# Kernel optimization log

Measured on AMD Instinct MI355X. Metric: run time of the kernel, lower is better.

The kernel has to match this reference:

```python
import jax, jax.numpy as jnp
import numpy as np

NUM_NODES = 116
EMBED = 64
HIDDEN = 64
OUT_FEAT = 116


def mish(x):
    return x * jnp.tanh(jax.nn.softplus(x))


def sage_conv(x, src, dst, w_l, b_l, w_r, n):
    # PyG SAGEConv (mean aggr): out = lin_l(mean_{j->i} x_j) + lin_r(x_i)
    agg = jax.ops.segment_sum(x[src], dst, num_segments=n)
    cnt = jax.ops.segment_sum(jnp.ones((src.shape[0],), x.dtype), dst, num_segments=n)
    mean = agg / jnp.clip(cnt, 1.0)[:, None]
    return mean @ w_l.T + b_l + x @ w_r.T


def setup_inputs() -> dict:
    key = jax.random.key(0)
    ks = jax.random.split(key, 12)
    B = 64
    N = B * NUM_NODES          # 7424 total nodes
    E = N * 32                 # 237568 edges
    d_in = EMBED * NUM_NODES   # 7424
    d_hid = HIDDEN * NUM_NODES # 7424
    d_out = OUT_FEAT * NUM_NODES  # 13456

    def lin_w(k, fan_out, fan_in):
        s = 1.0 / np.sqrt(fan_in)
        return jax.random.uniform(k, (fan_out, fan_in), jnp.float32, -s, s)

    return {
        "z": jax.random.normal(ks[0], (N, EMBED), jnp.float32),
        "edge_index": jax.random.randint(ks[1], (2, E), 0, N, jnp.int64),
        "batch_size": B,
        "w1_l": lin_w(ks[2], EMBED, EMBED),
        "b1_l": jnp.zeros((EMBED,), jnp.float32),
        "w1_r": lin_w(ks[3], EMBED, EMBED),
        "w2_l": lin_w(ks[4], EMBED, EMBED),
        "b2_l": jnp.zeros((EMBED,), jnp.float32),
        "w2_r": lin_w(ks[5], EMBED, EMBED),
        "fc1_w": lin_w(ks[6], d_hid, d_in),
        "fc1_b": jax.random.uniform(ks[7], (d_hid,), jnp.float32, -1/np.sqrt(d_in), 1/np.sqrt(d_in)),
        "fc2_w": lin_w(ks[8], d_out, d_hid),
        "fc2_b": jax.random.uniform(ks[9], (d_out,), jnp.float32, -1/np.sqrt(d_hid), 1/np.sqrt(d_hid)),
    }


def reference(z, edge_index, batch_size, w1_l, b1_l, w1_r, w2_l, b2_l, w2_r,
              fc1_w, fc1_b, fc2_w, fc2_b):
    n = z.shape[0]
    src, dst = edge_index[0], edge_index[1]
    h = mish(sage_conv(z, src, dst, w1_l, b1_l, w1_r, n))
    h = mish(sage_conv(h, src, dst, w2_l, b2_l, w2_r, n))
    h_flat = h.reshape(batch_size, NUM_NODES * EMBED)
    hidden = mish(h_flat @ fc1_w.T + fc1_b)
    x_rec = (hidden @ fc2_w.T + fc2_b).reshape(batch_size, NUM_NODES, OUT_FEAT)
    # enforce symmetry, unit diagonal
    sym = 0.5 * (x_rec + jnp.swapaxes(x_rec, 1, 2))
    eye = jnp.eye(NUM_NODES, dtype=bool)[None]
    sym = jnp.where(eye, jnp.asarray(1.0, sym.dtype), sym)
    return sym.reshape(batch_size * NUM_NODES, OUT_FEAT)
```

## Files before the change

kernel.cpp:

```cpp
#include <hip/hip_runtime.h>
#include <math.h>

#define NODES_TOT 7424
#define EDGES     237568
#define BATCH     64
#define NN        116
#define KDIM      7424
#define N1        7424
#define N2        13456
#define KSPLIT    8
#define NKB       116

typedef __attribute__((ext_vector_type(8))) short bf16x8;
typedef __attribute__((ext_vector_type(4))) float f32x4;
typedef __attribute__((ext_vector_type(4))) short s16x4;

__device__ __forceinline__ float mish_f(float v) {
    float sp = fmaxf(v, 0.0f) + log1pf(expf(-fabsf(v)));
    return v * tanhf(sp);
}

__device__ __forceinline__ unsigned short bf_rne(float f) {
    unsigned u = __float_as_uint(f);
    u += 0x7fffu + ((u >> 16) & 1u);
    return (unsigned short)(u >> 16);
}

__global__ void zero_kernel(int* __restrict__ p, int n) {
    int i = blockIdx.x * 256 + threadIdx.x;
    if (i < n) p[i] = 0;
}

__global__ void hist_kernel(const int* __restrict__ dst, int* __restrict__ hist) {
    int e = blockIdx.x * 256 + threadIdx.x;
    if (e < EDGES) atomicAdd(&hist[dst[e]], 1);
}

__global__ void scan_kernel(const int* __restrict__ hist, int* __restrict__ row_start,
                            int* __restrict__ cursor) {
    __shared__ int s[1024];
    int t = threadIdx.x;
    int base = t * 8;
    int loc[8];
    int sum = 0;
    #pragma unroll
    for (int c = 0; c < 8; ++c) {
        int idx = base + c;
        int v = (idx < NODES_TOT) ? hist[idx] : 0;
        loc[c] = sum;
        sum += v;
    }
    s[t] = sum;
    __syncthreads();
    for (int off = 1; off < 1024; off <<= 1) {
        int v = (t >= off) ? s[t - off] : 0;
        __syncthreads();
        s[t] += v;
        __syncthreads();
    }
    int excl = s[t] - sum;
    #pragma unroll
    for (int c = 0; c < 8; ++c) {
        int idx = base + c;
        if (idx < NODES_TOT) {
            int r = excl + loc[c];
            row_start[idx] = r;
            cursor[idx] = r;
        }
    }
}

__global__ void csr_fill_kernel(const int* __restrict__ src, const int* __restrict__ dst,
                                int* __restrict__ cursor, int* __restrict__ csr_src) {
    int e = blockIdx.x * 256 + threadIdx.x;
    if (e < EDGES) {
        int p = atomicAdd(&cursor[dst[e]], 1);
        csr_src[p] = src[e];
    }
}

template <bool BF>
__global__ void __launch_bounds__(256) conv_kernel(
        const float* __restrict__ x, const int* __restrict__ csr_src,
        const int* __restrict__ row_start, const int* __restrict__ deg_arr,
        const float* __restrict__ w_l, const float* __restrict__ b_l,
        const float* __restrict__ w_r, void* __restrict__ h_out_v) {
    __shared__ float wlT[64 * 64];
    __shared__ float wrT[64 * 64];
    __shared__ float mv[4][64];
    __shared__ float xv[4][64];
    int t = threadIdx.x;
    for (int i = 0; i < 16; ++i) {
        int idx = t + i * 256;
        int f = idx >> 6, k = idx & 63;
        wlT[k * 64 + f] = w_l[idx];
        wrT[k * 64 + f] = w_r[idx];
    }
    int g = t >> 6, f = t & 63;
    __syncthreads();
    for (int nb = blockIdx.x * 4; nb < NODES_TOT; nb += gridDim.x * 4) {
        int node = nb + g;
        int deg = deg_arr[node];
        int rs = row_start[node];
        float sum = 0.f;
        for (int e = 0; e < deg; ++e) {
            int s = csr_src[rs + e];
            sum += x[s * 64 + f];
        }
        float mean = sum / (float)max(deg, 1);
        mv[g][f] = mean;
        xv[g][f] = x[node * 64 + f];
        __syncthreads();
        float o = b_l[f];
        #pragma unroll
        for (int k = 0; k < 64; ++k) {
            o = fmaf(mv[g][k], wlT[k * 64 + f], o);
            o = fmaf(xv[g][k], wrT[k * 64 + f], o);
        }
        float m = mish_f(o);
        if (BF) ((unsigned short*)h_out_v)[node * 64 + f] = bf_rne(m);
        else    ((float*)h_out_v)[node * 64 + f] = m;
        __syncthreads();
    }
}

__global__ void __launch_bounds__(256) gemm_tile(
        const unsigned short* __restrict__ Abf, const float* __restrict__ W,
        float* __restrict__ Cp, int N) {
    __shared__ __align__(16) short Whi[512 * 8];
    __shared__ __align__(16) short Wlo[512 * 8];
    __shared__ __align__(16) short Ash[512 * 8];
    int t = threadIdx.x;
    int bx = blockIdx.x, by = blockIdx.y;
    int kb0 = (by * NKB) >> 3;
    int kb1 = ((by + 1) * NKB) >> 3;
    int n0 = bx * 64;
    int srow = t >> 2;
    int scq = t & 3;
    int wr = n0 + srow; if (wr >= N) wr = N - 1;
    const float* wsrc = W + (size_t)wr * KDIM + scq * 16;
    const unsigned short* asrc = Abf + (size_t)srow * KDIM + scq * 16;
    int f0 = scq * 2, f1 = f0 + 1;
    int c0 = (f0 * 64 + (srow ^ (f0 & 7))) * 8;
    int c1 = (f1 * 64 + (srow ^ (f1 & 7))) * 8;
    int wv = t >> 6, l = t & 63, l15 = l & 15, hi = l >> 4;
    f32x4 acc[4];
    #pragma unroll
    for (int g = 0; g < 4; ++g) acc[g] = (f32x4){0.f, 0.f, 0.f, 0.f};

    size_t k0 = (size_t)kb0 * 64;
    f32x4 w0 = *(const f32x4*)(wsrc + k0);
    f32x4 w1 = *(const f32x4*)(wsrc + k0 + 4);
    f32x4 w2 = *(const f32x4*)(wsrc + k0 + 8);
    f32x4 w3 = *(const f32x4*)(wsrc + k0 + 12);
    bf16x8 a0 = *(const bf16x8*)(asrc + k0);
    bf16x8 a1 = *(const bf16x8*)(asrc + k0 + 8);

    for (int kb = kb0; kb < kb1; ++kb) {
        bf16x8 h0, l0, h1, l1;
        #pragma unroll
        for (int j = 0; j < 4; ++j) {
            float fv = w0[j];
            unsigned short h = bf_rne(fv);
            h0[j] = (short)h;
            l0[j] = (short)bf_rne(fv - __uint_as_float((unsigned)h << 16));
            fv = w1[j];
            h = bf_rne(fv);
            h0[4 + j] = (short)h;
            l0[4 + j] = (short)bf_rne(fv - __uint_as_float((unsigned)h << 16));
            fv = w2[j];
            h = bf_rne(fv);
            h1[j] = (short)h;
            l1[j] = (short)bf_rne(fv - __uint_as_float((unsigned)h << 16));
            fv = w3[j];
            h = bf_rne(fv);
            h1[4 + j] = (short)h;
            l1[4 + j] = (short)bf_rne(fv - __uint_as_float((unsigned)h << 16));
        }
        __syncthreads();
        *(bf16x8*)&Whi[c0] = h0;
        *(bf16x8*)&Wlo[c0] = l0;
        *(bf16x8*)&Whi[c1] = h1;
        *(bf16x8*)&Wlo[c1] = l1;
        *(bf16x8*)&Ash[c0] = a0;
        *(bf16x8*)&Ash[c1] = a1;
        __syncthreads();
        if (kb + 1 < kb1) {
            size_t kn = (size_t)(kb + 1) * 64;
            w0 = *(const f32x4*)(wsrc + kn);
            w1 = *(const f32x4*)(wsrc + kn + 4);
            w2 = *(const f32x4*)(wsrc + kn + 8);
            w3 = *(const f32x4*)(wsrc + kn + 12);
            a0 = *(const bf16x8*)(asrc + kn);
            a1 = *(const bf16x8*)(asrc + kn + 8);
        }
        #pragma unroll
        for (int s = 0; s < 2; ++s) {
            int fw = s * 4 + hi;
            int wc = (fw * 64 + ((wv * 16 + l15) ^ (fw & 7))) * 8;
            bf16x8 bh = *(const bf16x8*)&Whi[wc];
            bf16x8 bl = *(const bf16x8*)&Wlo[wc];
            #pragma unroll
            for (int g = 0; g < 4; ++g) {
                int ac = (fw * 64 + ((g * 16 + l15) ^ (fw & 7))) * 8;
                bf16x8 av = *(const bf16x8*)&Ash[ac];
                acc[g] = __builtin_amdgcn_mfma_f32_16x16x32_bf16(av, bh, acc[g], 0, 0, 0);
                acc[g] = __builtin_amdgcn_mfma_f32_16x16x32_bf16(av, bl, acc[g], 0, 0, 0);
            }
        }
    }
    int gn = n0 + wv * 16 + l15;
    if (gn < N) {
        float* cp = Cp + (size_t)by * 64 * N;
        #pragma unroll
        for (int g = 0; g < 4; ++g)
            #pragma unroll
            for (int r = 0; r < 4; ++r)
                cp[(size_t)(g * 16 + hi * 4 + r) * N + gn] = acc[g][r];
    }
}

__global__ void reduce1_kernel(const float* __restrict__ Cp, const float* __restrict__ b,
                               unsigned short* __restrict__ A2) {
    int i4 = (blockIdx.x * 256 + threadIdx.x) * 4;
    if (i4 >= BATCH * N1) return;
    int n = i4 % N1;
    f32x4 acc = *(const f32x4*)(b + n);
    #pragma unroll
    for (int s = 0; s < KSPLIT; ++s)
        acc += *(const f32x4*)(Cp + (size_t)s * BATCH * N1 + i4);
    s16x4 o;
    #pragma unroll
    for (int j = 0; j < 4; ++j) o[j] = (short)bf_rne(mish_f(acc[j]));
    *(s16x4*)(A2 + i4) = o;
}

__global__ void reduce2_kernel(const float* __restrict__ Cp, const float* __restrict__ b,
                               float* __restrict__ C2) {
    int i4 = (blockIdx.x * 256 + threadIdx.x) * 4;
    if (i4 >= BATCH * N2) return;
    int n = i4 % N2;
    f32x4 acc = *(const f32x4*)(b + n);
    #pragma unroll
    for (int s = 0; s < KSPLIT; ++s)
        acc += *(const f32x4*)(Cp + (size_t)s * BATCH * N2 + i4);
    *(f32x4*)(C2 + i4) = acc;
}

__global__ void sym_kernel(const float* __restrict__ C2, float* __restrict__ out) {
    int tid = blockIdx.x * 256 + threadIdx.x;
    if (tid >= BATCH * NN * NN) return;
    int j = tid % NN;
    int r = tid / NN;
    int i = r % NN;
    int b = r / NN;
    float v;
    if (i == j) {
        v = 1.0f;
    } else {
        v = 0.5f * (C2[(size_t)b * N2 + i * NN + j] + C2[(size_t)b * N2 + j * NN + i]);
    }
    out[tid] = v;
}

extern "C" void kernel_launch(void* const* d_in, const int* in_sizes, int n_in,
                              void* d_out, int out_size, void* d_ws, size_t ws_size,
                              hipStream_t stream) {
    const float* z     = (const float*)d_in[0];
    const int*   edge  = (const int*)d_in[1];
    const float* w1_l  = (const float*)d_in[3];
    const float* b1_l  = (const float*)d_in[4];
    const float* w1_r  = (const float*)d_in[5];
    const float* w2_l  = (const float*)d_in[6];
    const float* b2_l  = (const float*)d_in[7];
    const float* w2_r  = (const float*)d_in[8];
    const float* fc1_w = (const float*)d_in[9];
    const float* fc1_b = (const float*)d_in[10];
    const float* fc2_w = (const float*)d_in[11];
    const float* fc2_b = (const float*)d_in[12];
    float* out = (float*)d_out;

    char* ws = (char*)d_ws;
    size_t off = 0;
    auto alloc = [&](size_t bytes) {
        void* p = ws + off;
        off = (off + bytes + 255) & ~(size_t)255;
        return p;
    };
    int*            hist      = (int*)alloc(NODES_TOT * 4);
    int*            row_start = (int*)alloc(NODES_TOT * 4);
    int*            cursor    = (int*)alloc(NODES_TOT * 4);
    int*            csr_src   = (int*)alloc((size_t)EDGES * 4);
    float*          h1        = (float*)alloc((size_t)NODES_TOT * 64 * 4);
    unsigned short* A1        = (unsigned short*)alloc((size_t)NODES_TOT * 64 * 2);
    float*          Cp1       = (float*)alloc((size_t)KSPLIT * BATCH * N1 * 4);
    unsigned short* A2        = (unsigned short*)alloc((size_t)BATCH * N1 * 2);
    float*          Cp2       = (float*)alloc((size_t)KSPLIT * BATCH * N2 * 4);
    float*          C2        = (float*)alloc((size_t)BATCH * N2 * 4);

    const int* src = edge;
    const int* dst = edge + EDGES;

    zero_kernel<<<(NODES_TOT + 255) / 256, 256, 0, stream>>>(hist, NODES_TOT);
    hist_kernel<<<(EDGES + 255) / 256, 256, 0, stream>>>(dst, hist);
    scan_kernel<<<1, 1024, 0, stream>>>(hist, row_start, cursor);
    csr_fill_kernel<<<(EDGES + 255) / 256, 256, 0, stream>>>(src, dst, cursor, csr_src);

    conv_kernel<false><<<928, 256, 0, stream>>>(z, csr_src, row_start, hist, w1_l, b1_l, w1_r, h1);
    conv_kernel<true><<<928, 256, 0, stream>>>(h1, csr_src, row_start, hist, w2_l, b2_l, w2_r, A1);

    gemm_tile<<<dim3(N1 / 64, KSPLIT), 256, 0, stream>>>(A1, fc1_w, Cp1, N1);
    reduce1_kernel<<<(BATCH * N1 / 4 + 255) / 256, 256, 0, stream>>>(Cp1, fc1_b, A2);

    gemm_tile<<<dim3((N2 + 63) / 64, KSPLIT), 256, 0, stream>>>(A2, fc2_w, Cp2, N2);
    reduce2_kernel<<<(BATCH * N2 / 4 + 255) / 256, 256, 0, stream>>>(Cp2, fc2_b, C2);

    sym_kernel<<<(BATCH * NN * NN + 255) / 256, 256, 0, stream>>>(C2, out);
}
```

Measured before the change: 329.9 us.

## Drop split-bf16 weight correction, read A from global, raise fc1 K-split

The GEMM tiles stop splitting each fp32 weight into hi and lo bf16 parts and run one MFMA per product instead of two. The A operand is no longer staged in shared memory and is read straight from global memory inside the MFMA loop. The weight staging layout changes to a plain unswizzled one, and fc1 now uses a 16-way K-split instead of 8. This halves MFMA work and shared memory use, but lowers weight precision to plain bf16 and may cause bank conflicts and more global loads for A.

```diff
diff --git a/kernel.cpp b/kernel.cpp
--- a/kernel.cpp
+++ b/kernel.cpp
@@ -8,8 +8,9 @@
 #define KDIM      7424
 #define N1        7424
 #define N2        13456
-#define KSPLIT    8
 #define NKB       116
+#define KSPLIT1   16
+#define KSPLIT2   8
 
 typedef __attribute__((ext_vector_type(8))) short bf16x8;
 typedef __attribute__((ext_vector_type(4))) float f32x4;
@@ -124,88 +125,57 @@
     }
 }
 
+template <int KSHIFT>
 __global__ void __launch_bounds__(256) gemm_tile(
         const unsigned short* __restrict__ Abf, const float* __restrict__ W,
         float* __restrict__ Cp, int N) {
-    __shared__ __align__(16) short Whi[512 * 8];
-    __shared__ __align__(16) short Wlo[512 * 8];
-    __shared__ __align__(16) short Ash[512 * 8];
+    __shared__ __align__(16) short Wsh[512 * 8];
     int t = threadIdx.x;
     int bx = blockIdx.x, by = blockIdx.y;
-    int kb0 = (by * NKB) >> 3;
-    int kb1 = ((by + 1) * NKB) >> 3;
+    int kb0 = (by * NKB) >> KSHIFT;
+    int kb1 = ((by + 1) * NKB) >> KSHIFT;
     int n0 = bx * 64;
-    int srow = t >> 2;
-    int scq = t & 3;
-    int wr = n0 + srow; if (wr >= N) wr = N - 1;
-    const float* wsrc = W + (size_t)wr * KDIM + scq * 16;
-    const unsigned short* asrc = Abf + (size_t)srow * KDIM + scq * 16;
-    int f0 = scq * 2, f1 = f0 + 1;
-    int c0 = (f0 * 64 + (srow ^ (f0 & 7))) * 8;
-    int c1 = (f1 * 64 + (srow ^ (f1 & 7))) * 8;
+    int r = t >> 2, q = t & 3;
+    int wr = n0 + r; if (wr >= N) wr = N - 1;
+    const float* wsrc = W + (size_t)wr * KDIM + q * 4;
+    int half = q & 1;
+    int fbase = q >> 1;
     int wv = t >> 6, l = t & 63, l15 = l & 15, hi = l >> 4;
     f32x4 acc[4];
     #pragma unroll
     for (int g = 0; g < 4; ++g) acc[g] = (f32x4){0.f, 0.f, 0.f, 0.f};
 
-    size_t k0 = (size_t)kb0 * 64;
-    f32x4 w0 = *(const f32x4*)(wsrc + k0);
-    f32x4 w1 = *(const f32x4*)(wsrc + k0 + 4);
-    f32x4 w2 = *(const f32x4*)(wsrc + k0 + 8);
-    f32x4 w3 = *(const f32x4*)(wsrc + k0 + 12);
-    bf16x8 a0 = *(const bf16x8*)(asrc + k0);
-    bf16x8 a1 = *(const bf16x8*)(asrc + k0 + 8);
-
+    f32x4 w[4];
+    {
+        size_t k0 = (size_t)kb0 * 64;
+        #pragma unroll
+        for (int i = 0; i < 4; ++i) w[i] = *(const f32x4*)(wsrc + k0 + i * 16);
+    }
     for (int kb = kb0; kb < kb1; ++kb) {
-        bf16x8 h0, l0, h1, l1;
-        #pragma unroll
-        for (int j = 0; j < 4; ++j) {
-            float fv = w0[j];
-            unsigned short h = bf_rne(fv);
-            h0[j] = (short)h;
-            l0[j] = (short)bf_rne(fv - __uint_as_float((unsigned)h << 16));
-            fv = w1[j];
-            h = bf_rne(fv);
-            h0[4 + j] = (short)h;
-            l0[4 + j] = (short)bf_rne(fv - __uint_as_float((unsigned)h << 16));
-            fv = w2[j];
-            h = bf_rne(fv);
-            h1[j] = (short)h;
-            l1[j] = (short)bf_rne(fv - __uint_as_float((unsigned)h << 16));
-            fv = w3[j];
-            h = bf_rne(fv);
-            h1[4 + j] = (short)h;
-            l1[4 + j] = (short)bf_rne(fv - __uint_as_float((unsigned)h << 16));
-        }
-        __syncthreads();
-        *(bf16x8*)&Whi[c0] = h0;
-        *(bf16x8*)&Wlo[c0] = l0;
-        *(bf16x8*)&Whi[c1] = h1;
-        *(bf16x8*)&Wlo[c1] = l1;
-        *(bf16x8*)&Ash[c0] = a0;
-        *(bf16x8*)&Ash[c1] = a1;
+        s16x4 cv[4];
+        #pragma unroll
+        for (int i = 0; i < 4; ++i)
+            #pragma unroll
+            for (int j = 0; j < 4; ++j) cv[i][j] = (short)bf_rne(w[i][j]);
+        __syncthreads();
+        #pragma unroll
+        for (int i = 0; i < 4; ++i)
+            *(s16x4*)&Wsh[((i * 2 + fbase) * 64 + r) * 8 + half * 4] = cv[i];
         __syncthreads();
         if (kb + 1 < kb1) {
             size_t kn = (size_t)(kb + 1) * 64;
-            w0 = *(const f32x4*)(wsrc + kn);
-            w1 = *(const f32x4*)(wsrc + kn + 4);
-            w2 = *(const f32x4*)(wsrc + kn + 8);
-            w3 = *(const f32x4*)(wsrc + kn + 12);
-            a0 = *(const bf16x8*)(asrc + kn);
-            a1 = *(const bf16x8*)(asrc + kn + 8);
-        }
+            #pragma unroll
+            for (int i = 0; i < 4; ++i) w[i] = *(const f32x4*)(wsrc + kn + i * 16);
+        }
+        size_t k0 = (size_t)kb * 64;
         #pragma unroll
         for (int s = 0; s < 2; ++s) {
             int fw = s * 4 + hi;
-            int wc = (fw * 64 + ((wv * 16 + l15) ^ (fw & 7))) * 8;
-            bf16x8 bh = *(const bf16x8*)&Whi[wc];
-            bf16x8 bl = *(const bf16x8*)&Wlo[wc];
+            bf16x8 bh = *(const bf16x8*)&Wsh[(fw * 64 + wv * 16 + l15) * 8];
             #pragma unroll
             for (int g = 0; g < 4; ++g) {
-                int ac = (fw * 64 + ((g * 16 + l15) ^ (fw & 7))) * 8;
-                bf16x8 av = *(const bf16x8*)&Ash[ac];
+                bf16x8 av = *(const bf16x8*)(Abf + (size_t)(g * 16 + l15) * KDIM + k0 + fw * 8);
                 acc[g] = __builtin_amdgcn_mfma_f32_16x16x32_bf16(av, bh, acc[g], 0, 0, 0);
-                acc[g] = __builtin_amdgcn_mfma_f32_16x16x32_bf16(av, bl, acc[g], 0, 0, 0);
             }
         }
     }
@@ -215,8 +185,8 @@
         #pragma unroll
         for (int g = 0; g < 4; ++g)
             #pragma unroll
-            for (int r = 0; r < 4; ++r)
-                cp[(size_t)(g * 16 + hi * 4 + r) * N + gn] = acc[g][r];
+            for (int rr = 0; rr < 4; ++rr)
+                cp[(size_t)(g * 16 + hi * 4 + rr) * N + gn] = acc[g][rr];
     }
 }
 
@@ -227,7 +197,7 @@
     int n = i4 % N1;
     f32x4 acc = *(const f32x4*)(b + n);
     #pragma unroll
-    for (int s = 0; s < KSPLIT; ++s)
+    for (int s = 0; s < KSPLIT1; ++s)
         acc += *(const f32x4*)(Cp + (size_t)s * BATCH * N1 + i4);
     s16x4 o;
     #pragma unroll
@@ -242,7 +212,7 @@
     int n = i4 % N2;
     f32x4 acc = *(const f32x4*)(b + n);
     #pragma unroll
-    for (int s = 0; s < KSPLIT; ++s)
+    for (int s = 0; s < KSPLIT2; ++s)
         acc += *(const f32x4*)(Cp + (size_t)s * BATCH * N2 + i4);
     *(f32x4*)(C2 + i4) = acc;
 }
@@ -293,9 +263,9 @@
     int*            csr_src   = (int*)alloc((size_t)EDGES * 4);
     float*          h1        = (float*)alloc((size_t)NODES_TOT * 64 * 4);
     unsigned short* A1        = (unsigned short*)alloc((size_t)NODES_TOT * 64 * 2);
-    float*          Cp1       = (float*)alloc((size_t)KSPLIT * BATCH * N1 * 4);
+    float*          Cp1       = (float*)alloc((size_t)KSPLIT1 * BATCH * N1 * 4);
     unsigned short* A2        = (unsigned short*)alloc((size_t)BATCH * N1 * 2);
-    float*          Cp2       = (float*)alloc((size_t)KSPLIT * BATCH * N2 * 4);
+    float*          Cp2       = (float*)alloc((size_t)KSPLIT2 * BATCH * N2 * 4);
     float*          C2        = (float*)alloc((size_t)BATCH * N2 * 4);
 
     const int* src = edge;
@@ -309,10 +279,10 @@
     conv_kernel<false><<<928, 256, 0, stream>>>(z, csr_src, row_start, hist, w1_l, b1_l, w1_r, h1);
     conv_kernel<true><<<928, 256, 0, stream>>>(h1, csr_src, row_start, hist, w2_l, b2_l, w2_r, A1);
 
-    gemm_tile<<<dim3(N1 / 64, KSPLIT), 256, 0, stream>>>(A1, fc1_w, Cp1, N1);
+    gemm_tile<4><<<dim3(N1 / 64, KSPLIT1), 256, 0, stream>>>(A1, fc1_w, Cp1, N1);
     reduce1_kernel<<<(BATCH * N1 / 4 + 255) / 256, 256, 0, stream>>>(Cp1, fc1_b, A2);
 
-    gemm_tile<<<dim3((N2 + 63) / 64, KSPLIT), 256, 0, stream>>>(A2, fc2_w, Cp2, N2);
+    gemm_tile<3><<<dim3((N2 + 63) / 64, KSPLIT2), 256, 0, stream>>>(A2, fc2_w, Cp2, N2);
     reduce2_kernel<<<(BATCH * N2 / 4 + 255) / 256, 256, 0, stream>>>(Cp2, fc2_b, C2);
 
     sym_kernel<<<(BATCH * NN * NN + 255) / 256, 256, 0, stream>>>(C2, out);
```

Measured after the change: 390.4 us. 1.18x slower.
